# Kernel optimization log

Hardware: AMD Instinct MI355X
Metric: run time of the kernel (lower is better)

The kernel has to match this reference:

```python
import jax, jax.numpy as jnp
import numpy as np

BINS = 10
LOSS_WEIGHT = 1.0


def setup_inputs() -> dict:
    key = jax.random.key(0)
    k1, k2, k3 = jax.random.split(key, 3)
    N, C = 524288, 80
    pred = jax.random.normal(k1, (N, C), dtype=jnp.float32)
    target = jax.random.randint(k2, (N, C), 0, 2, dtype=jnp.int32)
    weight = (jax.random.uniform(k3, (N, C)) < 0.9).astype(jnp.float32)
    return {"pred": pred, "target": target, "weight": weight}


def reference(pred, target, weight):
    tgt = target.astype(jnp.float32)
    valid = weight > 0
    # tot comes from .item() in torch -> plain constant scalar
    tot = jnp.maximum(valid.sum().astype(jnp.float32), 1.0)

    # gradient norm g = |sigmoid(pred).detach() - target| in [0, 1]
    g = jnp.abs(jax.nn.sigmoid(jax.lax.stop_gradient(pred)) - tgt)
    # edges are i/BINS with last edge 1+1e-6, so bin = floor(g*BINS) clipped to BINS-1
    bin_idx = jnp.clip((g * BINS).astype(jnp.int32), 0, BINS - 1)

    # per-bin count of valid samples (fused histogram instead of per-bin loop)
    counts = jax.ops.segment_sum(
        valid.ravel().astype(jnp.float32), bin_idx.ravel(), num_segments=BINS
    )
    n_nonempty = jnp.maximum((counts > 0).sum().astype(jnp.float32), 1.0)
    per_bin_w = jnp.where(counts > 0, tot / jnp.maximum(counts, 1.0), 0.0) / n_nonempty

    ghm_w = jnp.where(valid, per_bin_w[bin_idx], 0.0)
    ghm_w = jax.lax.stop_gradient(ghm_w)  # weights are detached in torch

    # binary_cross_entropy_with_logits, stable form
    bce = jnp.maximum(pred, 0.0) - pred * tgt + jnp.log1p(jnp.exp(-jnp.abs(pred)))
    # weight_reduce_loss: loss = (loss * weight).sum() / avg_factor (avg_factor=tot)
    loss = (bce * ghm_w * weight).sum() / tot
    return loss * LOSS_WEIGHT
```

## Files before the change

kernel.cpp:

```cpp
#include <hip/hip_runtime.h>
#include <math.h>

#define NBINS 10

__global__ __launch_bounds__(256) void ghmc_partials(
    const float* __restrict__ pred,
    const int*   __restrict__ target,
    const float* __restrict__ weight,
    float* __restrict__ ws_sum,
    int*   __restrict__ ws_cnt,
    long long n, int NB)
{
  float sum[NBINS];
  int   cnt[NBINS];
#pragma unroll
  for (int b = 0; b < NBINS; b++) { sum[b] = 0.0f; cnt[b] = 0; }

  const long long nv4    = n >> 2;
  const long long stride = (long long)gridDim.x * blockDim.x;
  long long idx = (long long)blockIdx.x * blockDim.x + threadIdx.x;

  const float4* p4 = (const float4*)pred;
  const int4*   t4 = (const int4*)target;
  const float4* w4 = (const float4*)weight;

  for (long long i = idx; i < nv4; i += stride) {
    float4 p = p4[i];
    int4   t = t4[i];
    float4 w = w4[i];
#pragma unroll
    for (int j = 0; j < 4; j++) {
      float pj = (&p.x)[j];
      float tj = (float)((&t.x)[j]);
      float wj = (&w.x)[j];
      float q = __expf(-fabsf(pj));
      float r = __builtin_amdgcn_rcpf(1.0f + q);
      float arg = (1.0f - 2.0f * tj) * pj;
      float g = (arg >= 0.0f) ? r : (q * r);
      float bce = fmaxf(pj, 0.0f) - pj * tj + __logf(1.0f + q);
      int bin = (wj > 0.0f) ? min((int)(g * 10.0f), NBINS - 1) : -1;
#pragma unroll
      for (int b = 0; b < NBINS; b++) {
        bool m = (bin == b);
        cnt[b] += m ? 1 : 0;
        sum[b] += m ? bce : 0.0f;
      }
    }
  }

  if (idx == 0) {
    for (long long i = (nv4 << 2); i < n; i++) {
      float pj = pred[i];
      float tj = (float)target[i];
      float wj = weight[i];
      float q = __expf(-fabsf(pj));
      float r = __builtin_amdgcn_rcpf(1.0f + q);
      float arg = (1.0f - 2.0f * tj) * pj;
      float g = (arg >= 0.0f) ? r : (q * r);
      float bce = fmaxf(pj, 0.0f) - pj * tj + __logf(1.0f + q);
      int bin = (wj > 0.0f) ? min((int)(g * 10.0f), NBINS - 1) : -1;
#pragma unroll
      for (int b = 0; b < NBINS; b++) {
        bool m = (bin == b);
        cnt[b] += m ? 1 : 0;
        sum[b] += m ? bce : 0.0f;
      }
    }
  }

  __shared__ float s_sum[NBINS];
  __shared__ int   s_cnt[NBINS];
  if (threadIdx.x < NBINS) { s_sum[threadIdx.x] = 0.0f; s_cnt[threadIdx.x] = 0; }
  __syncthreads();
  int lane = threadIdx.x & 63;
#pragma unroll
  for (int b = 0; b < NBINS; b++) {
    float v = sum[b];
    int   c = cnt[b];
    for (int off = 32; off >= 1; off >>= 1) {
      v += __shfl_down(v, off);
      c += __shfl_down(c, off);
    }
    if (lane == 0) {
      atomicAdd(&s_sum[b], v);
      atomicAdd(&s_cnt[b], c);
    }
  }
  __syncthreads();
  if (threadIdx.x < NBINS) {
    ws_sum[threadIdx.x * NB + blockIdx.x] = s_sum[threadIdx.x];
    ws_cnt[threadIdx.x * NB + blockIdx.x] = s_cnt[threadIdx.x];
  }
}

__global__ __launch_bounds__(256) void ghmc_finalize(
    const float* __restrict__ ws_sum,
    const int*   __restrict__ ws_cnt,
    float* __restrict__ out, int NB)
{
  float ls[NBINS];
  int   lc[NBINS];
#pragma unroll
  for (int b = 0; b < NBINS; b++) { ls[b] = 0.0f; lc[b] = 0; }

  for (int i = threadIdx.x; i < NB; i += 256) {
#pragma unroll
    for (int b = 0; b < NBINS; b++) {
      ls[b] += ws_sum[b * NB + i];
      lc[b] += ws_cnt[b * NB + i];
    }
  }

  __shared__ float ssum[NBINS][4];
  __shared__ int   scnt[NBINS][4];
  int lane = threadIdx.x & 63, wid = threadIdx.x >> 6;
#pragma unroll
  for (int b = 0; b < NBINS; b++) {
    float v = ls[b];
    int   c = lc[b];
    for (int off = 32; off >= 1; off >>= 1) {
      v += __shfl_down(v, off);
      c += __shfl_down(c, off);
    }
    if (lane == 0) { ssum[b][wid] = v; scnt[b][wid] = c; }
  }
  __syncthreads();

  if (threadIdx.x == 0) {
    int n_ne = 0;
    float sums[NBINS];
    float cnts[NBINS];
#pragma unroll
    for (int b = 0; b < NBINS; b++) {
      float v = 0.0f;
      int   c = 0;
      for (int w = 0; w < 4; w++) { v += ssum[b][w]; c += scnt[b][w]; }
      sums[b] = v;
      cnts[b] = (float)c;
      n_ne += (c > 0) ? 1 : 0;
    }
    float nne = (n_ne > 0) ? (float)n_ne : 1.0f;
    float loss = 0.0f;
#pragma unroll
    for (int b = 0; b < NBINS; b++) {
      if (cnts[b] > 0.0f) loss += sums[b] / (cnts[b] * nne);
    }
    out[0] = loss;
  }
}

extern "C" void kernel_launch(void* const* d_in, const int* in_sizes, int n_in,
                              void* d_out, int out_size, void* d_ws, size_t ws_size,
                              hipStream_t stream)
{
  const float* pred   = (const float*)d_in[0];
  const int*   target = (const int*)d_in[1];
  const float* weight = (const float*)d_in[2];
  float* out = (float*)d_out;
  long long n = (long long)in_sizes[0];

  int NB = 2048;
  size_t per_block = (size_t)NBINS * (sizeof(float) + sizeof(int));
  if (ws_size < (size_t)NB * per_block) {
    int maxnb = (int)(ws_size / per_block);
    NB = (maxnb < 1) ? 1 : maxnb;
  }
  float* ws_sum = (float*)d_ws;
  int*   ws_cnt = (int*)((char*)d_ws + (size_t)NBINS * NB * sizeof(float));

  ghmc_partials<<<NB, 256, 0, stream>>>(pred, target, weight, ws_sum, ws_cnt, n, NB);
  ghmc_finalize<<<1, 256, 0, stream>>>(ws_sum, ws_cnt, out, NB);
}
```

Measured before the change: 114.0 us.

## Bin via logit thresholds with cumulative ballot counts instead of sigmoid binning

Replaces the sigmoid-based bin index with comparisons of a signed logit against precomputed logit thresholds, accumulating cumulative (≥ threshold) sums and wave-level ballot popcounts. Per-bin values are then recovered by differencing adjacent cumulative bins. This removes the reciprocal, the float-to-int conversion and the per-bin equality masks, and replaces per-lane integer counters with scalar popcounts. The main loop is unrolled by two, the finalize kernel now uses double precision, and the shared-memory atomics are replaced with a per-wave staging array. Cumulative float sums that are differenced can lose precision, and threshold comparisons on the logit may disagree with the reference binning at bin edges.

```diff
diff --git a/kernel.cpp b/kernel.cpp
--- a/kernel.cpp
+++ b/kernel.cpp
@@ -2,19 +2,25 @@
 #include <math.h>
 
 #define NBINS 10
+#define NTH 9
+
 
 __global__ __launch_bounds__(256) void ghmc_partials(
     const float* __restrict__ pred,
     const int*   __restrict__ target,
     const float* __restrict__ weight,
-    float* __restrict__ ws_sum,
-    int*   __restrict__ ws_cnt,
+    float*        __restrict__ ws_sum,
+    unsigned int* __restrict__ ws_cnt,
     long long n, int NB)
 {
-  float sum[NBINS];
-  int   cnt[NBINS];
+  const float th[NTH] = { -2.1972246f, -1.3862944f, -0.84729786f, -0.40546511f,
+                           0.0f,
+                           0.40546511f, 0.84729786f, 1.3862944f,  2.1972246f };
+
+  float        T[NBINS];
+  unsigned int C[NBINS];
 #pragma unroll
-  for (int b = 0; b < NBINS; b++) { sum[b] = 0.0f; cnt[b] = 0; }
+  for (int b = 0; b < NBINS; b++) { T[b] = 0.0f; C[b] = 0u; }
 
   const long long nv4    = n >> 2;
   const long long stride = (long long)gridDim.x * blockDim.x;
@@ -24,100 +30,103 @@
   const int4*   t4 = (const int4*)target;
   const float4* w4 = (const float4*)weight;
 
-  for (long long i = idx; i < nv4; i += stride) {
+  auto proc = [&](float pj, int tj, float wj) {
+    float x     = (tj != 0) ? -pj : pj;
+    bool  valid = wj > 0.0f;
+    float xg    = valid ? x : -3.0e30f;
+    float q     = __expf(-fabsf(x));
+    float bce   = fmaxf(x, 0.0f) + __logf(1.0f + q);
+    bce *= wj;
+    T[0] += bce;
+    C[0] += (unsigned)__popcll(__ballot(valid));
+#pragma unroll
+    for (int k = 0; k < NTH; k++) {
+      bool c = xg >= th[k];
+      C[k + 1] += (unsigned)__popcll(__ballot(c));
+      T[k + 1] += c ? bce : 0.0f;
+    }
+  };
+
+  auto body = [&](long long i) {
     float4 p = p4[i];
     int4   t = t4[i];
     float4 w = w4[i];
 #pragma unroll
-    for (int j = 0; j < 4; j++) {
-      float pj = (&p.x)[j];
-      float tj = (float)((&t.x)[j]);
-      float wj = (&w.x)[j];
-      float q = __expf(-fabsf(pj));
-      float r = __builtin_amdgcn_rcpf(1.0f + q);
-      float arg = (1.0f - 2.0f * tj) * pj;
-      float g = (arg >= 0.0f) ? r : (q * r);
-      float bce = fmaxf(pj, 0.0f) - pj * tj + __logf(1.0f + q);
-      int bin = (wj > 0.0f) ? min((int)(g * 10.0f), NBINS - 1) : -1;
-#pragma unroll
-      for (int b = 0; b < NBINS; b++) {
-        bool m = (bin == b);
-        cnt[b] += m ? 1 : 0;
-        sum[b] += m ? bce : 0.0f;
-      }
-    }
+    for (int j = 0; j < 4; j++)
+      proc((&p.x)[j], (&t.x)[j], (&w.x)[j]);
+  };
+
+  long long i = idx;
+  for (; i + stride < nv4; i += 2 * stride) {
+    body(i);
+    body(i + stride);
+  }
+  if (i < nv4) body(i);
+
+  if (idx == 0) {
+    for (long long e = (nv4 << 2); e < n; e++)
+      proc(pred[e], target[e], weight[e]);
   }
 
-  if (idx == 0) {
-    for (long long i = (nv4 << 2); i < n; i++) {
-      float pj = pred[i];
-      float tj = (float)target[i];
-      float wj = weight[i];
-      float q = __expf(-fabsf(pj));
-      float r = __builtin_amdgcn_rcpf(1.0f + q);
-      float arg = (1.0f - 2.0f * tj) * pj;
-      float g = (arg >= 0.0f) ? r : (q * r);
-      float bce = fmaxf(pj, 0.0f) - pj * tj + __logf(1.0f + q);
-      int bin = (wj > 0.0f) ? min((int)(g * 10.0f), NBINS - 1) : -1;
+  float        S[NBINS];
+  unsigned int cnt[NBINS];
 #pragma unroll
-      for (int b = 0; b < NBINS; b++) {
-        bool m = (bin == b);
-        cnt[b] += m ? 1 : 0;
-        sum[b] += m ? bce : 0.0f;
-      }
-    }
+  for (int b = 0; b < NBINS; b++) {
+    float        tn = (b + 1 < NBINS) ? T[b + 1] : 0.0f;
+    unsigned int cn = (b + 1 < NBINS) ? C[b + 1] : 0u;
+    S[b]   = T[b] - tn;
+    cnt[b] = C[b] - cn;
   }
 
-  __shared__ float s_sum[NBINS];
-  __shared__ int   s_cnt[NBINS];
-  if (threadIdx.x < NBINS) { s_sum[threadIdx.x] = 0.0f; s_cnt[threadIdx.x] = 0; }
-  __syncthreads();
-  int lane = threadIdx.x & 63;
+  int lane = threadIdx.x & 63, wid = threadIdx.x >> 6;
 #pragma unroll
   for (int b = 0; b < NBINS; b++) {
-    float v = sum[b];
-    int   c = cnt[b];
-    for (int off = 32; off >= 1; off >>= 1) {
-      v += __shfl_down(v, off);
-      c += __shfl_down(c, off);
-    }
-    if (lane == 0) {
-      atomicAdd(&s_sum[b], v);
-      atomicAdd(&s_cnt[b], c);
-    }
+    float v = S[b];
+    for (int off = 32; off >= 1; off >>= 1) v += __shfl_down(v, off);
+    S[b] = v;
+  }
+
+  __shared__ float        ls[NBINS][4];
+  __shared__ unsigned int lc[NBINS][4];
+  if (lane == 0) {
+#pragma unroll
+    for (int b = 0; b < NBINS; b++) { ls[b][wid] = S[b]; lc[b][wid] = cnt[b]; }
   }
   __syncthreads();
   if (threadIdx.x < NBINS) {
-    ws_sum[threadIdx.x * NB + blockIdx.x] = s_sum[threadIdx.x];
-    ws_cnt[threadIdx.x * NB + blockIdx.x] = s_cnt[threadIdx.x];
+    int b = threadIdx.x;
+    float        s = ls[b][0] + ls[b][1] + ls[b][2] + ls[b][3];
+    unsigned int c = lc[b][0] + lc[b][1] + lc[b][2] + lc[b][3];
+    ws_sum[b * NB + blockIdx.x] = s;
+    ws_cnt[b * NB + blockIdx.x] = c;
   }
 }
 
 __global__ __launch_bounds__(256) void ghmc_finalize(
-    const float* __restrict__ ws_sum,
-    const int*   __restrict__ ws_cnt,
+    const float*        __restrict__ ws_sum,
+    const unsigned int* __restrict__ ws_cnt,
     float* __restrict__ out, int NB)
 {
-  float ls[NBINS];
-  int   lc[NBINS];
+  double    ds[NBINS];
+  long long dc[NBINS];
 #pragma unroll
-  for (int b = 0; b < NBINS; b++) { ls[b] = 0.0f; lc[b] = 0; }
+  for (int b = 0; b < NBINS; b++) { ds[b] = 0.0; dc[b] = 0; }
 
   for (int i = threadIdx.x; i < NB; i += 256) {
 #pragma unroll
     for (int b = 0; b < NBINS; b++) {
-      ls[b] += ws_sum[b * NB + i];
-      lc[b] += ws_cnt[b * NB + i];
+      ds[b] += (double)ws_sum[b * NB + i];
+      dc[b] += (long long)ws_cnt[b * NB + i];
     }
   }
 
-  __shared__ float ssum[NBINS][4];
-  __shared__ int   scnt[NBINS][4];
+  __shared__ double    ssum[NBINS][4];
+  __shared__ long long scnt[NBINS][4];
   int lane = threadIdx.x & 63, wid = threadIdx.x >> 6;
 #pragma unroll
   for (int b = 0; b < NBINS; b++) {
-    float v = ls[b];
-    int   c = lc[b];
+    double    v = ds[b];
+    long long c = dc[b];
     for (int off = 32; off >= 1; off >>= 1) {
       v += __shfl_down(v, off);
       c += __shfl_down(c, off);
@@ -128,24 +137,22 @@
 
   if (threadIdx.x == 0) {
     int n_ne = 0;
-    float sums[NBINS];
-    float cnts[NBINS];
+    double sums[NBINS];
+    long long cnts[NBINS];
 #pragma unroll
     for (int b = 0; b < NBINS; b++) {
-      float v = 0.0f;
-      int   c = 0;
+      double v = 0.0; long long c = 0;
       for (int w = 0; w < 4; w++) { v += ssum[b][w]; c += scnt[b][w]; }
-      sums[b] = v;
-      cnts[b] = (float)c;
+      sums[b] = v; cnts[b] = c;
       n_ne += (c > 0) ? 1 : 0;
     }
-    float nne = (n_ne > 0) ? (float)n_ne : 1.0f;
-    float loss = 0.0f;
+    double nne  = (n_ne > 0) ? (double)n_ne : 1.0;
+    double loss = 0.0;
 #pragma unroll
     for (int b = 0; b < NBINS; b++) {
-      if (cnts[b] > 0.0f) loss += sums[b] / (cnts[b] * nne);
+      if (cnts[b] > 0) loss += sums[b] / ((double)cnts[b] * nne);
     }
-    out[0] = loss;
+    out[0] = (float)loss;
   }
 }
 
@@ -160,13 +167,13 @@
   long long n = (long long)in_sizes[0];
 
   int NB = 2048;
-  size_t per_block = (size_t)NBINS * (sizeof(float) + sizeof(int));
+  size_t per_block = (size_t)NBINS * (sizeof(float) + sizeof(unsigned int));
   if (ws_size < (size_t)NB * per_block) {
     int maxnb = (int)(ws_size / per_block);
     NB = (maxnb < 1) ? 1 : maxnb;
   }
-  float* ws_sum = (float*)d_ws;
-  int*   ws_cnt = (int*)((char*)d_ws + (size_t)NBINS * NB * sizeof(float));
+  float*        ws_sum = (float*)d_ws;
+  unsigned int* ws_cnt = (unsigned int*)((char*)d_ws + (size_t)NBINS * NB * sizeof(float));
 
   ghmc_partials<<<NB, 256, 0, stream>>>(pred, target, weight, ws_sum, ws_cnt, n, NB);
   ghmc_finalize<<<1, 256, 0, stream>>>(ws_sum, ws_cnt, out, NB);
```

After: 124.7 us. +9.4%, slower.
